# Performance work log

Hardware: AMD Instinct MI355X
Metric: run time of the kernel (lower is better)

Reference implementation:

```python
import jax, jax.numpy as jnp
import numpy as np

B, S, D, H, FF = 2, 2048, 1024, 16, 4096
HD = D // H
SCALE = 1.0 / np.sqrt(HD).astype(np.float32)
EPS = 1e-5


def _ln(x, g, b):
    m = jnp.mean(x, axis=-1, keepdims=True)
    v = jnp.mean((x - m) ** 2, axis=-1, keepdims=True)
    return (x - m) * jax.lax.rsqrt(v + EPS) * g + b


def setup_inputs() -> dict:
    key = jax.random.key(0)
    ks = jax.random.split(key, 8)
    def lin(k, fan_in, shape):
        return (jax.random.normal(k, shape, jnp.float32) / np.sqrt(fan_in)).astype(jnp.float32)
    return {
        "x": jax.random.normal(ks[0], (B, S, D), jnp.float32),
        "w_qkv": lin(ks[1], D, (D, 3 * D)),          # qkv_proj (no bias)
        "w_o": lin(ks[2], D, (D, D)),                 # out_proj
        "b_o": jnp.zeros((D,), jnp.float32),
        "g1": jnp.ones((D,), jnp.float32),            # attn LayerNorm
        "bt1": jnp.zeros((D,), jnp.float32),
        "w1": lin(ks[3], D, (D, FF)),                 # FFN linear1
        "b1": jnp.zeros((FF,), jnp.float32),
        "w2": lin(ks[4], FF, (FF, D)),                # FFN linear2
        "b2": jnp.zeros((D,), jnp.float32),
        "g2": jnp.ones((D,), jnp.float32),            # FFN LayerNorm
        "bt2": jnp.zeros((D,), jnp.float32),
    }


def reference(x, w_qkv, w_o, b_o, g1, bt1, w1, b1, w2, b2, g2, bt2):
    # --- MultiHeadAttention (post-LN, dropout=eval/identity) ---
    qkv = (x @ w_qkv).reshape(B, S, H, 3 * HD)
    q, k, v = jnp.split(qkv, 3, axis=-1)  # each [B,S,H,HD]
    # kernel_func = scaled softmax over keys
    scores = jnp.einsum("bihd,bjhd->bhij", q, k) * SCALE  # [B,H,S,S]
    attn = jax.nn.softmax(scores, axis=-1)
    ao = jnp.einsum("bhij,bjhd->bihd", attn, v).reshape(B, S, D)
    y = _ln(x + ao @ w_o + b_o, g1, bt1)
    # --- FFN (post-LN) ---
    h = jax.nn.relu(y @ w1 + b1)
    return _ln(y + h @ w2 + b2, g2, bt2)
```

## Files before the change

### kernel.cpp

```cpp
#include <hip/hip_runtime.h>
#include <hip/hip_bf16.h>

#define B_  2
#define S_  2048
#define D_  1024
#define H_  16
#define HD_ 64
#define FF_ 4096
#define NT  (B_ * S_)
#define SCALE_ 0.125f
#define KLOG2E 0.1803368801111f
#define EPS_  1e-5f

typedef __attribute__((ext_vector_type(8))) short bf16x8;
typedef __attribute__((ext_vector_type(4))) float f32x4;

__device__ inline short f2bf(float f) {
    __hip_bfloat16 h = __float2bfloat16(f);
    return __builtin_bit_cast(short, h);
}
__device__ inline float bf2f(unsigned short u) {
    __hip_bfloat16 h = __builtin_bit_cast(__hip_bfloat16, u);
    return __bfloat162float(h);
}
__device__ inline unsigned int pk2bf(float lo, float hi) {
    __hip_bfloat162 h = __float22bfloat162_rn(float2{lo, hi});
    const unsigned short l16 = __builtin_bit_cast(unsigned short, h.x);
    const unsigned short h16 = __builtin_bit_cast(unsigned short, h.y);
    return (unsigned int)l16 | ((unsigned int)h16 << 16);
}

#define GLOBAL_AS __attribute__((address_space(1)))
#define LDS_AS    __attribute__((address_space(3)))

struct DetectArgs { const unsigned short* p[12]; int n[12]; };

__global__ __launch_bounds__(256) void detect_kernel(DetectArgs a, int* flags) {
    const int t = blockIdx.x;
    const unsigned short* s = a.p[t];
    const int cnt = min(a.n[t], 16384);
    const int tid = threadIdx.x;
    int huge = 0, zeven = 0;
    for (int i = tid; i < cnt; i += 256) {
        const unsigned short v = s[i];
        const int e = (v >> 7) & 0xFF;
        if (e >= 142) huge++;
        if (((i & 1) == 0) && ((v & 0x7FFF) == 0)) zeven++;
    }
    __shared__ int sh, sz;
    if (tid == 0) { sh = 0; sz = 0; }
    __syncthreads();
    atomicAdd(&sh, huge);
    atomicAdd(&sz, zeven);
    __syncthreads();
    if (tid == 0) flags[t] = (sh > 0 || sz * 4 > cnt) ? 1 : 0;
}

struct VecArgs { const void* src[7]; float* dst[7]; int n[7]; int fidx[7]; };

__global__ __launch_bounds__(256) void conv_x_vecs_kernel(
    const void* __restrict__ src, unsigned short* __restrict__ dst, int n,
    VecArgs a, const int* __restrict__ flags)
{
    const int i = blockIdx.x * 256 + threadIdx.x;
    if (i < n) {
        if (flags[0])
            dst[i] = (unsigned short)f2bf(((const float*)src)[i]);
        else
            dst[i] = ((const unsigned short*)src)[i];
    }
    if (blockIdx.x < 7) {
        const int v = blockIdx.x;
        const int f = flags[a.fidx[v]];
        for (int j = threadIdx.x; j < a.n[v]; j += 256) {
            a.dst[v][j] = f ? ((const float*)a.src[v])[j]
                            : bf2f(((const unsigned short*)a.src[v])[j]);
        }
    }
}

struct TArgs {
    const void* src[4]; unsigned short* dst[4];
    int K[4], N[4], fidx[4], start[5];
};

__global__ __launch_bounds__(256) void conv_t_all_kernel(
    TArgs t, const int* __restrict__ flags)
{
    __shared__ short T[32][33];
    const int tile = blockIdx.x;
    int w = 0;
    if (tile >= t.start[1]) w = 1;
    if (tile >= t.start[2]) w = 2;
    if (tile >= t.start[3]) w = 3;
    const int rel = tile - t.start[w];
    const int K = t.K[w], N = t.N[w];
    const int tilesN = N / 32;
    const int kt = (rel / tilesN) * 32, nt = (rel % tilesN) * 32;
    const void* src = t.src[w];
    unsigned short* dst = t.dst[w];
    const int f = flags[t.fidx[w]];

    const int c  = threadIdx.x & 31;
    const int r0 = (threadIdx.x >> 5) * 4;
#pragma unroll
    for (int i = 0; i < 4; i++) {
        const int r = r0 + i;
        const size_t gi = (size_t)(kt + r) * N + nt + c;
        short v = f ? f2bf(((const float*)src)[gi])
                    : (short)((const unsigned short*)src)[gi];
        T[c][r] = v;
    }
    __syncthreads();
#pragma unroll
    for (int i = 0; i < 4; i++) {
        const int n = r0 + i;
        dst[(size_t)(nt + n) * K + kt + c] = (unsigned short)T[n][c];
    }
}

template<bool HAS_BIAS, bool RELU, int RES, bool OUT_F32, bool QSCALE>
__global__ __launch_bounds__(256) void gemm128_kernel(
    const unsigned short* __restrict__ A,
    const unsigned short* __restrict__ Bt,
    const float* __restrict__ bias,
    const unsigned short* __restrict__ resb,
    const float* __restrict__ resf,
    const int* __restrict__ flags,
    void* __restrict__ out,
    int M, int N, int K)
{
    __shared__ short As[2][128 * 32];
    __shared__ short Bs[2][128 * 32];

    const int tid  = threadIdx.x;
    const int wave = tid >> 6;
    const int lane = tid & 63;
    const int quad = lane >> 4;
    const int l16  = lane & 15;

    const int row0 = blockIdx.x * 128;
    const int col0 = blockIdx.y * 128;

    const int ldrow = lane >> 2;
    const int ldk   = (lane & 3) * 8;
    const unsigned short* agp0 = A  + (size_t)(row0 + wave * 32 + ldrow) * K + ldk;
    const unsigned short* agp1 = agp0 + (size_t)16 * K;
    const unsigned short* bgp0 = Bt + (size_t)(col0 + wave * 32 + ldrow) * K + ldk;
    const unsigned short* bgp1 = bgp0 + (size_t)16 * K;

    const int wm = (wave >> 1) * 64;
    const int wn = (wave & 1) * 64;

    f32x4 acc[4][4] = {};

    for (int k0 = 0; k0 < K; k0 += 64) {
#pragma unroll
        for (int h = 0; h < 2; h++) {
            __builtin_amdgcn_global_load_lds(
                (const GLOBAL_AS void*)(agp0 + k0 + h * 32),
                (LDS_AS void*)&As[h][wave * 1024 + lane * 8], 16, 0, 0);
            __builtin_amdgcn_global_load_lds(
                (const GLOBAL_AS void*)(agp1 + k0 + h * 32),
                (LDS_AS void*)&As[h][wave * 1024 + 512 + lane * 8], 16, 0, 0);
            __builtin_amdgcn_global_load_lds(
                (const GLOBAL_AS void*)(bgp0 + k0 + h * 32),
                (LDS_AS void*)&Bs[h][wave * 1024 + lane * 8], 16, 0, 0);
            __builtin_amdgcn_global_load_lds(
                (const GLOBAL_AS void*)(bgp1 + k0 + h * 32),
                (LDS_AS void*)&Bs[h][wave * 1024 + 512 + lane * 8], 16, 0, 0);
        }
        __syncthreads();

#pragma unroll
        for (int h = 0; h < 2; h++) {
            bf16x8 af[4], bfr[4];
#pragma unroll
            for (int mi = 0; mi < 4; mi++)
                af[mi] = *reinterpret_cast<const bf16x8*>(
                    &As[h][(wm + mi * 16 + l16) * 32 + quad * 8]);
#pragma unroll
            for (int ni = 0; ni < 4; ni++)
                bfr[ni] = *reinterpret_cast<const bf16x8*>(
                    &Bs[h][(wn + ni * 16 + l16) * 32 + quad * 8]);
#pragma unroll
            for (int mi = 0; mi < 4; mi++)
#pragma unroll
                for (int ni = 0; ni < 4; ni++)
                    acc[mi][ni] = __builtin_amdgcn_mfma_f32_16x16x32_bf16(
                        af[mi], bfr[ni], acc[mi][ni], 0, 0, 0);
        }
        __syncthreads();
    }

    int resIsF32 = 0;
    if constexpr (RES == 2) resIsF32 = flags[0];

#pragma unroll
    for (int ni = 0; ni < 4; ni++) {
        const int col = col0 + wn + ni * 16 + l16;
        float badd = 0.f;
        if constexpr (HAS_BIAS) badd = bias[col];
        float qs = 1.f;
        if constexpr (QSCALE)
            qs = (((col0 + wn + ni * 16) % 192) < 64) ? KLOG2E : 1.f;
#pragma unroll
        for (int mi = 0; mi < 4; mi++) {
#pragma unroll
            for (int r = 0; r < 4; r++) {
                const int row = row0 + wm + mi * 16 + quad * 4 + r;
                float v = acc[mi][ni][r] + badd;
                if constexpr (QSCALE) v *= qs;
                if constexpr (RES == 1) {
                    v += bf2f(resb[(size_t)row * N + col]);
                } else if constexpr (RES == 2) {
                    v += resIsF32 ? resf[(size_t)row * N + col]
                                  : bf2f(resb[(size_t)row * N + col]);
                }
                if constexpr (RELU) v = fmaxf(v, 0.f);
                if constexpr (OUT_F32)
                    ((float*)out)[(size_t)row * N + col] = v;
                else
                    ((unsigned short*)out)[(size_t)row * N + col] =
                        (unsigned short)f2bf(v);
            }
        }
    }
}

__global__ __launch_bounds__(256) void gemm128_sk_kernel(
    const unsigned short* __restrict__ A,
    const unsigned short* __restrict__ Bt,
    float* __restrict__ out0,
    float* __restrict__ out1,
    int M, int N, int K)
{
    __shared__ short As[2][128 * 32];
    __shared__ short Bs[2][128 * 32];

    const int tid  = threadIdx.x;
    const int wave = tid >> 6;
    const int lane = tid & 63;
    const int quad = lane >> 4;
    const int l16  = lane & 15;

    const int row0 = blockIdx.x * 128;
    const int col0 = blockIdx.y * 128;
    const int z    = blockIdx.z;
    const int Kh   = K >> 1;

    const unsigned short* Az  = A  + (size_t)z * Kh;
    const unsigned short* Btz = Bt + (size_t)z * Kh;
    float* out = z ? out1 : out0;

    const int ldrow = lane >> 2;
    const int ldk   = (lane & 3) * 8;
    const unsigned short* agp0 = Az  + (size_t)(row0 + wave * 32 + ldrow) * K + ldk;
    const unsigned short* agp1 = agp0 + (size_t)16 * K;
    const unsigned short* bgp0 = Btz + (size_t)(col0 + wave * 32 + ldrow) * K + ldk;
    const unsigned short* bgp1 = bgp0 + (size_t)16 * K;

    const int wm = (wave >> 1) * 64;
    const int wn = (wave & 1) * 64;

    f32x4 acc[4][4] = {};

    for (int k0 = 0; k0 < Kh; k0 += 64) {
#pragma unroll
        for (int h = 0; h < 2; h++) {
            __builtin_amdgcn_global_load_lds(
                (const GLOBAL_AS void*)(agp0 + k0 + h * 32),
                (LDS_AS void*)&As[h][wave * 1024 + lane * 8], 16, 0, 0);
            __builtin_amdgcn_global_load_lds(
                (const GLOBAL_AS void*)(agp1 + k0 + h * 32),
                (LDS_AS void*)&As[h][wave * 1024 + 512 + lane * 8], 16, 0, 0);
            __builtin_amdgcn_global_load_lds(
                (const GLOBAL_AS void*)(bgp0 + k0 + h * 32),
                (LDS_AS void*)&Bs[h][wave * 1024 + lane * 8], 16, 0, 0);
            __builtin_amdgcn_global_load_lds(
                (const GLOBAL_AS void*)(bgp1 + k0 + h * 32),
                (LDS_AS void*)&Bs[h][wave * 1024 + 512 + lane * 8], 16, 0, 0);
        }
        __syncthreads();

#pragma unroll
        for (int h = 0; h < 2; h++) {
            bf16x8 af[4], bfr[4];
#pragma unroll
            for (int mi = 0; mi < 4; mi++)
                af[mi] = *reinterpret_cast<const bf16x8*>(
                    &As[h][(wm + mi * 16 + l16) * 32 + quad * 8]);
#pragma unroll
            for (int ni = 0; ni < 4; ni++)
                bfr[ni] = *reinterpret_cast<const bf16x8*>(
                    &Bs[h][(wn + ni * 16 + l16) * 32 + quad * 8]);
#pragma unroll
            for (int mi = 0; mi < 4; mi++)
#pragma unroll
                for (int ni = 0; ni < 4; ni++)
                    acc[mi][ni] = __builtin_amdgcn_mfma_f32_16x16x32_bf16(
                        af[mi], bfr[ni], acc[mi][ni], 0, 0, 0);
        }
        __syncthreads();
    }

#pragma unroll
    for (int ni = 0; ni < 4; ni++) {
        const int col = col0 + wn + ni * 16 + l16;
#pragma unroll
        for (int mi = 0; mi < 4; mi++)
#pragma unroll
            for (int r = 0; r < 4; r++) {
                const int row = row0 + wm + mi * 16 + quad * 4 + r;
                out[(size_t)row * N + col] = acc[mi][ni][r];
            }
    }
}

__global__ __launch_bounds__(256) void attn_kernel(
    const unsigned short* __restrict__ qkv,
    unsigned short* __restrict__ ao)
{
    const int qt = blockIdx.x;
    const int h  = blockIdx.y;
    const int b  = blockIdx.z;

    const int tid  = threadIdx.x;
    const int wave = tid >> 6;
    const int lane = tid & 63;
    const int quad = lane >> 4;
    const int l16  = lane & 15;

    __shared__ short Ks[64 * 72];
    __shared__ short Vt[64 * 72];
    __shared__ short Ps[4 * 32 * 72];

    bf16x8 qf[2][2];
#pragma unroll
    for (int mi = 0; mi < 2; mi++) {
        const int qrow = qt * 128 + wave * 32 + mi * 16 + l16;
        const unsigned short* qb = qkv + (size_t)(b * S_ + qrow) * 3072 + h * 192;
        qf[mi][0] = *reinterpret_cast<const bf16x8*>(qb + quad * 8);
        qf[mi][1] = *reinterpret_cast<const bf16x8*>(qb + 32 + quad * 8);
    }

    bf16x8 vones;
#pragma unroll
    for (int j = 0; j < 8; j++) vones[j] = (short)0x3F80;

    f32x4 o[2][4] = {};
    f32x4 o_l[2] = {};

    const int skey = tid >> 3;
    const int soct = tid & 7;
    const int vp   = tid >> 3;
    const int kA   = (vp & 15) + ((vp >> 4) << 5);
    const int kB   = kA + 16;
    const int posA = 4 * (vp & 15) + 2 * (vp >> 4);
    const int vwr  = ((posA >> 3) ^ soct) * 8 + (posA & 7);

    const int pb = wave * (32 * 72);

    const unsigned short* kbase0 = qkv + (size_t)(b * S_) * 3072 + h * 192 + 64;
    const unsigned short* vbase0 = qkv + (size_t)(b * S_) * 3072 + h * 192 + 128;

    bf16x8 pk0 = *reinterpret_cast<const bf16x8*>(kbase0 + (size_t)skey * 3072 + soct * 8);
    bf16x8 pk1 = *reinterpret_cast<const bf16x8*>(kbase0 + (size_t)(skey + 32) * 3072 + soct * 8);
    bf16x8 pv0 = *reinterpret_cast<const bf16x8*>(vbase0 + (size_t)kA * 3072 + soct * 8);
    bf16x8 pv1 = *reinterpret_cast<const bf16x8*>(vbase0 + (size_t)kB * 3072 + soct * 8);

    for (int kb = 0; kb < S_; kb += 64) {
        {
            const int woct0 = soct ^ ((skey >> 3) & 1);
            *reinterpret_cast<bf16x8*>(&Ks[skey * 72 + woct0 * 8]) = pk0;
            const int woct1 = soct ^ (((skey + 32) >> 3) & 1);
            *reinterpret_cast<bf16x8*>(&Ks[(skey + 32) * 72 + woct1 * 8]) = pk1;
#pragma unroll
            for (int j = 0; j < 8; j++) {
                const int d = soct * 8 + j;
                const unsigned int val =
                    (unsigned int)(unsigned short)pv0[j] |
                    ((unsigned int)(unsigned short)pv1[j] << 16);
                *reinterpret_cast<unsigned int*>(&Vt[d * 72 + vwr]) = val;
            }
        }
        __syncthreads();

        {
            const int kbn = (kb + 64 < S_) ? kb + 64 : kb;
            pk0 = *reinterpret_cast<const bf16x8*>(
                kbase0 + (size_t)(kbn + skey) * 3072 + soct * 8);
            pk1 = *reinterpret_cast<const bf16x8*>(
                kbase0 + (size_t)(kbn + skey + 32) * 3072 + soct * 8);
            pv0 = *reinterpret_cast<const bf16x8*>(
                vbase0 + (size_t)(kbn + kA) * 3072 + soct * 8);
            pv1 = *reinterpret_cast<const bf16x8*>(
                vbase0 + (size_t)(kbn + kB) * 3072 + soct * 8);
        }

        f32x4 s[2][4] = {};
#pragma unroll
        for (int c2 = 0; c2 < 2; c2++) {
#pragma unroll
            for (int nt = 0; nt < 4; nt++) {
                const int key = nt * 16 + l16;
                const int roct = (c2 * 4 + quad) ^ ((key >> 3) & 1);
                bf16x8 kf = *reinterpret_cast<const bf16x8*>(
                    &Ks[key * 72 + roct * 8]);
                s[0][nt] = __builtin_amdgcn_mfma_f32_16x16x32_bf16(qf[0][c2], kf, s[0][nt], 0, 0, 0);
                s[1][nt] = __builtin_amdgcn_mfma_f32_16x16x32_bf16(qf[1][c2], kf, s[1][nt], 0, 0, 0);
            }
        }

#pragma unroll
        for (int mi = 0; mi < 2; mi++) {
#pragma unroll
            for (int r = 0; r < 4; r++) {
                const int m = mi * 16 + quad * 4 + r;
                const float p0 = exp2f(s[mi][0][r]);
                const float p1 = exp2f(s[mi][1][r]);
                const float p2 = exp2f(s[mi][2][r]);
                const float p3 = exp2f(s[mi][3][r]);
                uint2 w;
                w.x = pk2bf(p0, p1);
                w.y = pk2bf(p2, p3);
                *reinterpret_cast<uint2*>(&Ps[pb + m * 72 + l16 * 4]) = w;
            }
        }

#pragma unroll
        for (int c2 = 0; c2 < 2; c2++) {
            bf16x8 pf[2];
#pragma unroll
            for (int mi = 0; mi < 2; mi++) {
                const int m = mi * 16 + l16;
                pf[mi] = *reinterpret_cast<const bf16x8*>(
                    &Ps[pb + m * 72 + c2 * 32 + quad * 8]);
            }
#pragma unroll
            for (int ct = 0; ct < 4; ct++) {
                const int row = ct * 16 + l16;
                const int blk = (c2 * 4 + quad) ^ (row >> 3);
                bf16x8 vf = *reinterpret_cast<const bf16x8*>(
                    &Vt[row * 72 + blk * 8]);
                o[0][ct] = __builtin_amdgcn_mfma_f32_16x16x32_bf16(pf[0], vf, o[0][ct], 0, 0, 0);
                o[1][ct] = __builtin_amdgcn_mfma_f32_16x16x32_bf16(pf[1], vf, o[1][ct], 0, 0, 0);
            }
            o_l[0] = __builtin_amdgcn_mfma_f32_16x16x32_bf16(pf[0], vones, o_l[0], 0, 0, 0);
            o_l[1] = __builtin_amdgcn_mfma_f32_16x16x32_bf16(pf[1], vones, o_l[1], 0, 0, 0);
        }
        __syncthreads();
    }

#pragma unroll
    for (int mi = 0; mi < 2; mi++) {
        f32x4 rl;
#pragma unroll
        for (int r = 0; r < 4; r++) rl[r] = 1.f / o_l[mi][r];
#pragma unroll
        for (int ct = 0; ct < 4; ct++)
#pragma unroll
            for (int r = 0; r < 4; r++) {
                const int row = qt * 128 + wave * 32 + mi * 16 + quad * 4 + r;
                ao[(size_t)(b * S_ + row) * D_ + h * HD_ + ct * 16 + l16] =
                    (unsigned short)f2bf(o[mi][ct][r] * rl[r]);
            }
    }
}

template<int RESM, bool FLAG_OUT>
__global__ __launch_bounds__(256) void ln_sum_kernel(
    const float* __restrict__ p0,
    const float* __restrict__ p1,
    const float* __restrict__ bias,
    const unsigned short* __restrict__ resb,
    const float* __restrict__ resf,
    const float* __restrict__ g,
    const float* __restrict__ bt,
    const int* __restrict__ flags,
    void* __restrict__ out)
{
    const int row = blockIdx.x;
    const int tid = threadIdx.x;
    const int c0  = tid * 4;
    const size_t base = (size_t)row * D_ + c0;

    float4 a = *reinterpret_cast<const float4*>(p0 + base);
    float4 bq = *reinterpret_cast<const float4*>(p1 + base);
    float4 bi = *reinterpret_cast<const float4*>(bias + c0);

    float v[4] = {a.x + bq.x + bi.x, a.y + bq.y + bi.y,
                  a.z + bq.z + bi.z, a.w + bq.w + bi.w};

    if constexpr (RESM == 1) {
        if (flags[0]) {
            float4 rv = *reinterpret_cast<const float4*>(resf + base);
            v[0] += rv.x; v[1] += rv.y; v[2] += rv.z; v[3] += rv.w;
        } else {
            uint2 rv = *reinterpret_cast<const uint2*>(resb + base);
            v[0] += bf2f((unsigned short)(rv.x & 0xFFFF));
            v[1] += bf2f((unsigned short)(rv.x >> 16));
            v[2] += bf2f((unsigned short)(rv.y & 0xFFFF));
            v[3] += bf2f((unsigned short)(rv.y >> 16));
        }
    } else {
        uint2 rv = *reinterpret_cast<const uint2*>(resb + base);
        v[0] += bf2f((unsigned short)(rv.x & 0xFFFF));
        v[1] += bf2f((unsigned short)(rv.x >> 16));
        v[2] += bf2f((unsigned short)(rv.y & 0xFFFF));
        v[3] += bf2f((unsigned short)(rv.y >> 16));
    }

    float s = v[0] + v[1] + v[2] + v[3];
    float sq = v[0] * v[0] + v[1] * v[1] + v[2] * v[2] + v[3] * v[3];
#pragma unroll
    for (int msk = 1; msk < 64; msk <<= 1) {
        s += __shfl_xor(s, msk);
        sq += __shfl_xor(sq, msk);
    }
    __shared__ float ss[4], ssq[4];
    if ((tid & 63) == 0) { ss[tid >> 6] = s; ssq[tid >> 6] = sq; }
    __syncthreads();
    s = ss[0] + ss[1] + ss[2] + ss[3];
    sq = ssq[0] + ssq[1] + ssq[2] + ssq[3];

    const float mean = s * (1.f / D_);
    const float var = sq * (1.f / D_) - mean * mean;
    const float rinv = rsqrtf(var + EPS_);

    float w[4];
#pragma unroll
    for (int i = 0; i < 4; i++)
        w[i] = (v[i] - mean) * rinv * g[c0 + i] + bt[c0 + i];

    int outF32 = 0;
    if constexpr (FLAG_OUT) outF32 = flags[0];

    if (FLAG_OUT && outF32) {
        float4 o4 = {w[0], w[1], w[2], w[3]};
        *reinterpret_cast<float4*>((float*)out + base) = o4;
    } else {
        uint2 o2;
        o2.x = pk2bf(w[0], w[1]);
        o2.y = pk2bf(w[2], w[3]);
        *reinterpret_cast<uint2*>((unsigned short*)out + base) = o2;
    }
}

extern "C" void kernel_launch(void* const* d_in, const int* in_sizes, int n_in,
                              void* d_out, int out_size, void* d_ws, size_t ws_size,
                              hipStream_t stream) {
    char* ws = (char*)d_ws;

    int*            flags = (int*)(ws + 0);
    unsigned short* xb    = (unsigned short*)(ws + 256);
    unsigned short* wqkvT = (unsigned short*)(ws + 8388864);
    unsigned short* woT   = (unsigned short*)(ws + 14680320);
    unsigned short* w1T   = (unsigned short*)(ws + 16777472);
    unsigned short* w2T   = (unsigned short*)(ws + 25166080);
    float*          bof   = (float*)(ws + 33554688);
    float*          g1f   = (float*)(ws + 33558784);
    float*          bt1f  = (float*)(ws + 33562880);
    float*          b1f   = (float*)(ws + 33566976);
    float*          b2f   = (float*)(ws + 33583360);
    float*          g2f   = (float*)(ws + 33587456);
    float*          bt2f  = (float*)(ws + 33591552);
    unsigned short* qkv   = (unsigned short*)(ws + 33595648);
    unsigned short* ao    = (unsigned short*)(ws + 256);
    unsigned short* y     = (unsigned short*)(ws + 33595648);
    unsigned short* hbuf  = (unsigned short*)(ws + 41984256);
    float*          part0 = (float*)(ws + 58761472);
    float*          part1 = (float*)(ws + 75538688);
    float*          hpart0= (float*)(ws + 256);

    dim3 blk(256);

    DetectArgs da;
    for (int i = 0; i < 12; i++) {
        da.p[i] = (const unsigned short*)d_in[i];
        da.n[i] = in_sizes[i];
    }
    detect_kernel<<<dim3(12), blk, 0, stream>>>(da, flags);

    VecArgs va;
    const int vidx[7] = {3, 4, 5, 7, 9, 10, 11};
    float* vdst[7] = {bof, g1f, bt1f, b1f, b2f, g2f, bt2f};
    for (int i = 0; i < 7; i++) {
        va.src[i] = d_in[vidx[i]];
        va.dst[i] = vdst[i];
        va.n[i]   = in_sizes[vidx[i]];
        va.fidx[i] = vidx[i];
    }
    conv_x_vecs_kernel<<<dim3((NT * D_ + 255) / 256), blk, 0, stream>>>(
        d_in[0], xb, NT * D_, va, flags);

    TArgs ta;
    ta.src[0] = d_in[1]; ta.dst[0] = wqkvT; ta.K[0] = D_;  ta.N[0] = 3 * D_; ta.fidx[0] = 1;
    ta.src[1] = d_in[2]; ta.dst[1] = woT;   ta.K[1] = D_;  ta.N[1] = D_;     ta.fidx[1] = 2;
    ta.src[2] = d_in[6]; ta.dst[2] = w1T;   ta.K[2] = D_;  ta.N[2] = FF_;    ta.fidx[2] = 6;
    ta.src[3] = d_in[8]; ta.dst[3] = w2T;   ta.K[3] = FF_; ta.N[3] = D_;     ta.fidx[3] = 8;
    ta.start[0] = 0;
    for (int wI = 0; wI < 4; wI++)
        ta.start[wI + 1] = ta.start[wI] + (ta.K[wI] / 32) * (ta.N[wI] / 32);
    conv_t_all_kernel<<<dim3(ta.start[4]), blk, 0, stream>>>(ta, flags);

    gemm128_kernel<false, false, 0, false, true>
        <<<dim3(NT / 128, 3072 / 128), blk, 0, stream>>>(
            xb, wqkvT, nullptr, nullptr, nullptr, flags, qkv, NT, 3072, 1024);

    attn_kernel<<<dim3(S_ / 128, H_, B_), blk, 0, stream>>>(qkv, ao);

    gemm128_sk_kernel<<<dim3(NT / 128, 1024 / 128, 2), blk, 0, stream>>>(
        ao, woT, part0, part1, NT, 1024, 1024);

    ln_sum_kernel<1, false><<<dim3(NT), blk, 0, stream>>>(
        part0, part1, bof, (const unsigned short*)d_in[0], (const float*)d_in[0],
        g1f, bt1f, flags, y);

    gemm128_kernel<true, true, 0, false, false>
        <<<dim3(NT / 128, 4096 / 128), blk, 0, stream>>>(
            y, w1T, b1f, nullptr, nullptr, flags, hbuf, NT, 4096, 1024);

    gemm128_sk_kernel<<<dim3(NT / 128, 1024 / 128, 2), blk, 0, stream>>>(
        hbuf, w2T, hpart0, part1, NT, 1024, 4096);

    ln_sum_kernel<2, true><<<dim3(NT), blk, 0, stream>>>(
        hpart0, part1, b2f, y, nullptr, g2f, bt2f, flags, d_out);
}
```

Measured before the change: 394.0 us.

## Split attention key range across two wave groups per block and merge via LDS

Doubles the attention block to 512 threads, with two 4-wave groups each processing half of the key sequence for the same 128 queries, using dynamic shared memory. Partial unnormalized outputs and row sums from the second group are exchanged through LDS and added before normalization. This targets low occupancy and the long serial key loop given only 512 blocks, at the cost of more LDS, an extra reduction barrier and possible register pressure under the 512-thread bound.

```diff
diff --git a/kernel.cpp b/kernel.cpp
--- a/kernel.cpp
+++ b/kernel.cpp
@@ -317,28 +317,33 @@
     }
 }
 
-__global__ __launch_bounds__(256) void attn_kernel(
+__global__ __launch_bounds__(512) void attn_kernel(
     const unsigned short* __restrict__ qkv,
     unsigned short* __restrict__ ao)
 {
+    extern __shared__ char smem[];
+
     const int qt = blockIdx.x;
     const int h  = blockIdx.y;
     const int b  = blockIdx.z;
 
     const int tid  = threadIdx.x;
     const int wave = tid >> 6;
+    const int g    = wave >> 2;
+    const int gw   = wave & 3;
     const int lane = tid & 63;
     const int quad = lane >> 4;
     const int l16  = lane & 15;
-
-    __shared__ short Ks[64 * 72];
-    __shared__ short Vt[64 * 72];
-    __shared__ short Ps[4 * 32 * 72];
+    const int gtid = tid & 255;
+
+    short* Ks = (short*)smem + g * (64 * 72);
+    short* Vt = (short*)(smem + 18432) + g * (64 * 72);
+    short* Ps = (short*)(smem + 36864) + wave * (32 * 72);
 
     bf16x8 qf[2][2];
 #pragma unroll
     for (int mi = 0; mi < 2; mi++) {
-        const int qrow = qt * 128 + wave * 32 + mi * 16 + l16;
+        const int qrow = qt * 128 + gw * 32 + mi * 16 + l16;
         const unsigned short* qb = qkv + (size_t)(b * S_ + qrow) * 3072 + h * 192;
         qf[mi][0] = *reinterpret_cast<const bf16x8*>(qb + quad * 8);
         qf[mi][1] = *reinterpret_cast<const bf16x8*>(qb + 32 + quad * 8);
@@ -351,25 +356,26 @@
     f32x4 o[2][4] = {};
     f32x4 o_l[2] = {};
 
-    const int skey = tid >> 3;
-    const int soct = tid & 7;
-    const int vp   = tid >> 3;
+    const int skey = gtid >> 3;
+    const int soct = gtid & 7;
+    const int vp   = gtid >> 3;
     const int kA   = (vp & 15) + ((vp >> 4) << 5);
     const int kB   = kA + 16;
     const int posA = 4 * (vp & 15) + 2 * (vp >> 4);
     const int vwr  = ((posA >> 3) ^ soct) * 8 + (posA & 7);
 
-    const int pb = wave * (32 * 72);
+    const int kb0   = g * (S_ / 2);
+    const int kbend = kb0 + S_ / 2;
 
     const unsigned short* kbase0 = qkv + (size_t)(b * S_) * 3072 + h * 192 + 64;
     const unsigned short* vbase0 = qkv + (size_t)(b * S_) * 3072 + h * 192 + 128;
 
-    bf16x8 pk0 = *reinterpret_cast<const bf16x8*>(kbase0 + (size_t)skey * 3072 + soct * 8);
-    bf16x8 pk1 = *reinterpret_cast<const bf16x8*>(kbase0 + (size_t)(skey + 32) * 3072 + soct * 8);
-    bf16x8 pv0 = *reinterpret_cast<const bf16x8*>(vbase0 + (size_t)kA * 3072 + soct * 8);
-    bf16x8 pv1 = *reinterpret_cast<const bf16x8*>(vbase0 + (size_t)kB * 3072 + soct * 8);
-
-    for (int kb = 0; kb < S_; kb += 64) {
+    bf16x8 pk0 = *reinterpret_cast<const bf16x8*>(kbase0 + (size_t)(kb0 + skey) * 3072 + soct * 8);
+    bf16x8 pk1 = *reinterpret_cast<const bf16x8*>(kbase0 + (size_t)(kb0 + skey + 32) * 3072 + soct * 8);
+    bf16x8 pv0 = *reinterpret_cast<const bf16x8*>(vbase0 + (size_t)(kb0 + kA) * 3072 + soct * 8);
+    bf16x8 pv1 = *reinterpret_cast<const bf16x8*>(vbase0 + (size_t)(kb0 + kB) * 3072 + soct * 8);
+
+    for (int kb = kb0; kb < kbend; kb += 64) {
         {
             const int woct0 = soct ^ ((skey >> 3) & 1);
             *reinterpret_cast<bf16x8*>(&Ks[skey * 72 + woct0 * 8]) = pk0;
@@ -387,7 +393,7 @@
         __syncthreads();
 
         {
-            const int kbn = (kb + 64 < S_) ? kb + 64 : kb;
+            const int kbn = (kb + 64 < kbend) ? kb + 64 : kb;
             pk0 = *reinterpret_cast<const bf16x8*>(
                 kbase0 + (size_t)(kbn + skey) * 3072 + soct * 8);
             pk1 = *reinterpret_cast<const bf16x8*>(
@@ -424,7 +430,7 @@
                 uint2 w;
                 w.x = pk2bf(p0, p1);
                 w.y = pk2bf(p2, p3);
-                *reinterpret_cast<uint2*>(&Ps[pb + m * 72 + l16 * 4]) = w;
+                *reinterpret_cast<uint2*>(&Ps[m * 72 + l16 * 4]) = w;
             }
         }
 
@@ -435,7 +441,7 @@
             for (int mi = 0; mi < 2; mi++) {
                 const int m = mi * 16 + l16;
                 pf[mi] = *reinterpret_cast<const bf16x8*>(
-                    &Ps[pb + m * 72 + c2 * 32 + quad * 8]);
+                    &Ps[m * 72 + c2 * 32 + quad * 8]);
             }
 #pragma unroll
             for (int ct = 0; ct < 4; ct++) {
@@ -452,19 +458,43 @@
         __syncthreads();
     }
 
-#pragma unroll
-    for (int mi = 0; mi < 2; mi++) {
-        f32x4 rl;
-#pragma unroll
-        for (int r = 0; r < 4; r++) rl[r] = 1.f / o_l[mi][r];
-#pragma unroll
-        for (int ct = 0; ct < 4; ct++)
-#pragma unroll
-            for (int r = 0; r < 4; r++) {
-                const int row = qt * 128 + wave * 32 + mi * 16 + quad * 4 + r;
-                ao[(size_t)(b * S_ + row) * D_ + h * HD_ + ct * 16 + l16] =
-                    (unsigned short)f2bf(o[mi][ct][r] * rl[r]);
-            }
+    float* ex = (float*)smem;
+    const int slot = (gw * 64 + lane) * 40;
+    if (g == 1) {
+#pragma unroll
+        for (int mi = 0; mi < 2; mi++) {
+#pragma unroll
+            for (int ct = 0; ct < 4; ct++)
+                *reinterpret_cast<f32x4*>(&ex[slot + mi * 16 + ct * 4]) = o[mi][ct];
+            *reinterpret_cast<f32x4*>(&ex[slot + 32 + mi * 4]) = o_l[mi];
+        }
+    }
+    __syncthreads();
+    if (g == 0) {
+#pragma unroll
+        for (int mi = 0; mi < 2; mi++) {
+#pragma unroll
+            for (int ct = 0; ct < 4; ct++) {
+                f32x4 t = *reinterpret_cast<const f32x4*>(&ex[slot + mi * 16 + ct * 4]);
+                o[mi][ct] += t;
+            }
+            f32x4 tl = *reinterpret_cast<const f32x4*>(&ex[slot + 32 + mi * 4]);
+            o_l[mi] += tl;
+        }
+#pragma unroll
+        for (int mi = 0; mi < 2; mi++) {
+            f32x4 rl;
+#pragma unroll
+            for (int r = 0; r < 4; r++) rl[r] = 1.f / o_l[mi][r];
+#pragma unroll
+            for (int ct = 0; ct < 4; ct++)
+#pragma unroll
+                for (int r = 0; r < 4; r++) {
+                    const int row = qt * 128 + gw * 32 + mi * 16 + quad * 4 + r;
+                    ao[(size_t)(b * S_ + row) * D_ + h * HD_ + ct * 16 + l16] =
+                        (unsigned short)f2bf(o[mi][ct][r] * rl[r]);
+                }
+        }
     }
 }
 
@@ -575,6 +605,13 @@
 
     dim3 blk(256);
 
+    static int attn_attr_done = 0;
+    if (!attn_attr_done) {
+        hipFuncSetAttribute(reinterpret_cast<const void*>(attn_kernel),
+                            hipFuncAttributeMaxDynamicSharedMemorySize, 73728);
+        attn_attr_done = 1;
+    }
+
     DetectArgs da;
     for (int i = 0; i < 12; i++) {
         da.p[i] = (const unsigned short*)d_in[i];
@@ -608,7 +645,7 @@
         <<<dim3(NT / 128, 3072 / 128), blk, 0, stream>>>(
             xb, wqkvT, nullptr, nullptr, nullptr, flags, qkv, NT, 3072, 1024);
 
-    attn_kernel<<<dim3(S_ / 128, H_, B_), blk, 0, stream>>>(qkv, ao);
+    attn_kernel<<<dim3(S_ / 128, H_, B_), dim3(512), 73728, stream>>>(qkv, ao);
 
     gemm128_sk_kernel<<<dim3(NT / 128, 1024 / 128, 2), blk, 0, stream>>>(
         ao, woT, part0, part1, NT, 1024, 1024);
```

Result: faster. 385.9 us (-2.0%).
